# Optimization experiments

Measured on AMD Instinct MI355X. Metric: run time of the kernel, lower is better.

The kernel has to match this reference:

```python
import jax, jax.numpy as jnp
import numpy as np

EPS = 1e-05
B, T, F = 16, 2048, 768


def setup_inputs() -> dict:
    key = jax.random.key(0)
    k1, k2 = jax.random.split(key)
    input_values = jax.random.normal(k1, (B, T, F), dtype=jnp.float32)
    attention_mask = jax.random.randint(k2, (B, T), 0, 2, dtype=jnp.int32)
    return {"input_values": input_values, "attention_mask": attention_mask}


def _gauss_noise(shape):
    # mirrors _get_gauss_noise: scale randn into [0,1], then eps*((1-9)*g + 9)
    g = jax.random.normal(jax.random.key(42), shape, dtype=jnp.float32)
    g = g - jnp.min(g)
    g = g / jnp.max(g)
    return EPS * ((1.0 - 9.0) * g + 9.0)


def reference(input_values, attention_mask):
    x = input_values  # [B, T, F]
    Bx, Tx, Fx = x.shape
    # per-sample valid prefix length, as in the torch loop (vectorized)
    seq_lens = jnp.sum(attention_mask, axis=1).astype(jnp.float32)        # [B]
    rel = seq_lens / jnp.max(seq_lens)                                    # [B]
    actual = jnp.round(rel * Tx).astype(jnp.int32)                        # [B]
    # prefix mask over time: token t valid iff t < actual[b]
    m = (jnp.arange(Tx)[None, :] < actual[:, None]).astype(x.dtype)       # [B, T]
    cnt = actual.astype(x.dtype)[:, None]                                 # [B, 1]
    xm = x * m[:, :, None]
    mean = jnp.sum(xm, axis=1) / cnt                                      # [B, F]
    diff = (x - mean[:, None, :]) * m[:, :, None]
    # torch.std default: unbiased (ddof=1)
    std = jnp.sqrt(jnp.sum(diff * diff, axis=1) / (cnt - 1.0))            # [B, F]
    mean = mean + _gauss_noise(mean.shape)
    std = std + EPS
    pooled = jnp.concatenate([mean, std], axis=1)                         # [B, 2F]
    return pooled[:, None, :]                                             # [B, 1, 2F]
```

## Files before the change

kernel.cpp:

```cpp
#include <hip/hip_runtime.h>
#include <hip/hip_bf16.h>

#define B 16
#define T 2048
#define F 768
#define F4 (F / 4)
#define EPS 1e-5f
#define TS 64
#define TCHUNK (T / TS)


__global__ __launch_bounds__(1024) void k_actual(const int* __restrict__ mask,
                                                 int* __restrict__ actual) {
    __shared__ float slen[B];
    const int wave = threadIdx.x >> 6;
    const int lane = threadIdx.x & 63;
    int s = 0;
    const int* row = mask + wave * T;
    for (int t = lane; t < T; t += 64) s += row[t];
    for (int off = 32; off > 0; off >>= 1) s += __shfl_down(s, off, 64);
    if (lane == 0) slen[wave] = (float)s;
    __syncthreads();
    if (threadIdx.x < B) {
        float m = 0.f;
        for (int i = 0; i < B; i++) m = fmaxf(m, slen[i]);
        float rel = slen[threadIdx.x] / m;
        actual[threadIdx.x] = (int)rintf(rel * (float)T);
    }
}

__global__ __launch_bounds__(192) void k_partial(const float4* __restrict__ x,
                                                 const int* __restrict__ actual,
                                                 float* __restrict__ sum,
                                                 float* __restrict__ sumsq) {
    const int b = blockIdx.y;
    const int tstart = blockIdx.x * TCHUNK;
    const int tend = min(tstart + TCHUNK, actual[b]);
    const int tid = threadIdx.x;
    const float4* xb = x + (size_t)b * T * F4;

    float4 s = make_float4(0.f, 0.f, 0.f, 0.f);
    float4 q = make_float4(0.f, 0.f, 0.f, 0.f);
    for (int t = tstart; t < tend; ++t) {
        float4 v = xb[(size_t)t * F4 + tid];
        s.x += v.x; s.y += v.y; s.z += v.z; s.w += v.w;
        q.x += v.x * v.x; q.y += v.y * v.y; q.z += v.z * v.z; q.w += v.w * v.w;
    }
    if (tend > tstart) {
        const int base = b * F + 4 * tid;
        atomicAdd(&sum[base + 0], s.x);
        atomicAdd(&sum[base + 1], s.y);
        atomicAdd(&sum[base + 2], s.z);
        atomicAdd(&sum[base + 3], s.w);
        atomicAdd(&sumsq[base + 0], q.x);
        atomicAdd(&sumsq[base + 1], q.y);
        atomicAdd(&sumsq[base + 2], q.z);
        atomicAdd(&sumsq[base + 3], q.w);
    }
}

__global__ __launch_bounds__(256) void k_final(const float* __restrict__ sum,
                                               const float* __restrict__ sumsq,
                                               const int* __restrict__ actual,
                                               float* __restrict__ out) {
    const int idx = blockIdx.x * 256 + threadIdx.x;
    if (idx >= B * F) return;
    const int b = idx / F;
    const int f = idx - b * F;
    const float cnt = (float)actual[b];
    const float s = sum[idx];
    const float q = sumsq[idx];
    const float mean = s / cnt;
    float var = (q - s * s / cnt) / (cnt - 1.f);
    var = fmaxf(var, 0.f);
    out[b * 2 * F + f]     = mean;
    out[b * 2 * F + F + f] = sqrtf(var) + EPS;
}

extern "C" void kernel_launch(void* const* d_in, const int* in_sizes, int n_in,
                              void* d_out, int out_size, void* d_ws, size_t ws_size,
                              hipStream_t stream) {
    const float* x   = (const float*)d_in[0];
    const int* mask  = (const int*)d_in[1];
    float* out       = (float*)d_out;

    float* sum   = (float*)d_ws;
    float* sumsq = sum + B * F;
    int* actual  = (int*)(sumsq + B * F);

    hipMemsetAsync(d_ws, 0, (size_t)(2 * B * F) * sizeof(float), stream);

    k_actual<<<1, 1024, 0, stream>>>(mask, actual);
    k_partial<<<dim3(TS, B), 192, 0, stream>>>((const float4*)x, actual, sum, sumsq);
    k_final<<<(B * F + 255) / 256, 256, 0, stream>>>(sum, sumsq, actual, out);
}
```

Before: 170.0 us.

## Fuse mask-length computation into partial kernel and replace atomics with partial buffers

Drops the separate k_actual kernel and the memset. Each partial block now recomputes all 16 sequence lengths from the mask itself (128 KB read per block, mostly served from cache). The float atomics are replaced by plain per-tile partial-sum writes, and k_final reduces over the 64 tiles. This removes two launches and the atomic contention, in exchange for redundant mask reads in every block and an extra 2×64×B×F partial buffer that has to be written and read back.

Result: slower. 209.5 us (+23.2%).

```diff
diff --git a/kernel.cpp b/kernel.cpp
--- a/kernel.cpp
+++ b/kernel.cpp
@@ -8,35 +8,47 @@
 #define EPS 1e-5f
 #define TS 64
 #define TCHUNK (T / TS)
+#define NTHR 192
 
 
-__global__ __launch_bounds__(1024) void k_actual(const int* __restrict__ mask,
-                                                 int* __restrict__ actual) {
-    __shared__ float slen[B];
-    const int wave = threadIdx.x >> 6;
-    const int lane = threadIdx.x & 63;
-    int s = 0;
-    const int* row = mask + wave * T;
-    for (int t = lane; t < T; t += 64) s += row[t];
-    for (int off = 32; off > 0; off >>= 1) s += __shfl_down(s, off, 64);
-    if (lane == 0) slen[wave] = (float)s;
-    __syncthreads();
-    if (threadIdx.x < B) {
-        float m = 0.f;
-        for (int i = 0; i < B; i++) m = fmaxf(m, slen[i]);
-        float rel = slen[threadIdx.x] / m;
-        actual[threadIdx.x] = (int)rintf(rel * (float)T);
+__global__ __launch_bounds__(NTHR) void k_partial(const float4* __restrict__ x,
+                                                  const int* __restrict__ mask,
+                                                  float4* __restrict__ psum,
+                                                  float4* __restrict__ psq,
+                                                  int* __restrict__ actual_out) {
+    const int b    = blockIdx.y;
+    const int tile = blockIdx.x;
+    const int tid  = threadIdx.x;
+
+    __shared__ int red[12][16];
+    __shared__ int s_actual;
+    {
+        const int r = tid & 15;
+        const int j = tid >> 4;
+        int acc = 0;
+        const int* mrow = mask + r * T;
+        for (int t = j; t < T; t += 12) acc += mrow[t];
+        red[j][r] = acc;
+        __syncthreads();
+        if (tid < 16) {
+            int s = 0;
+            for (int j2 = 0; j2 < 12; j2++) s += red[j2][tid];
+            red[0][tid] = s;
+        }
+        __syncthreads();
+        if (tid == 0) {
+            float mx = 0.f;
+            for (int i = 0; i < B; i++) mx = fmaxf(mx, (float)red[0][i]);
+            float rel = (float)red[0][b] / mx;
+            s_actual = (int)rintf(rel * (float)T);
+        }
+        __syncthreads();
     }
-}
+    const int actual = s_actual;
+    if (tile == 0 && tid == 0) actual_out[b] = actual;
 
-__global__ __launch_bounds__(192) void k_partial(const float4* __restrict__ x,
-                                                 const int* __restrict__ actual,
-                                                 float* __restrict__ sum,
-                                                 float* __restrict__ sumsq) {
-    const int b = blockIdx.y;
-    const int tstart = blockIdx.x * TCHUNK;
-    const int tend = min(tstart + TCHUNK, actual[b]);
-    const int tid = threadIdx.x;
+    const int tstart = tile * TCHUNK;
+    const int tend   = min(tstart + TCHUNK, actual);
     const float4* xb = x + (size_t)b * T * F4;
 
     float4 s = make_float4(0.f, 0.f, 0.f, 0.f);
@@ -46,30 +58,25 @@
         s.x += v.x; s.y += v.y; s.z += v.z; s.w += v.w;
         q.x += v.x * v.x; q.y += v.y * v.y; q.z += v.z * v.z; q.w += v.w * v.w;
     }
-    if (tend > tstart) {
-        const int base = b * F + 4 * tid;
-        atomicAdd(&sum[base + 0], s.x);
-        atomicAdd(&sum[base + 1], s.y);
-        atomicAdd(&sum[base + 2], s.z);
-        atomicAdd(&sum[base + 3], s.w);
-        atomicAdd(&sumsq[base + 0], q.x);
-        atomicAdd(&sumsq[base + 1], q.y);
-        atomicAdd(&sumsq[base + 2], q.z);
-        atomicAdd(&sumsq[base + 3], q.w);
-    }
+    const size_t o = (size_t)(tile * B + b) * F4 + tid;
+    psum[o] = s;
+    psq[o]  = q;
 }
 
-__global__ __launch_bounds__(256) void k_final(const float* __restrict__ sum,
-                                               const float* __restrict__ sumsq,
+__global__ __launch_bounds__(256) void k_final(const float* __restrict__ psum,
+                                               const float* __restrict__ psq,
                                                const int* __restrict__ actual,
                                                float* __restrict__ out) {
     const int idx = blockIdx.x * 256 + threadIdx.x;
     if (idx >= B * F) return;
     const int b = idx / F;
     const int f = idx - b * F;
+    float s = 0.f, q = 0.f;
+    for (int tile = 0; tile < TS; ++tile) {
+        s += psum[(size_t)tile * B * F + idx];
+        q += psq [(size_t)tile * B * F + idx];
+    }
     const float cnt = (float)actual[b];
-    const float s = sum[idx];
-    const float q = sumsq[idx];
     const float mean = s / cnt;
     float var = (q - s * s / cnt) / (cnt - 1.f);
     var = fmaxf(var, 0.f);
@@ -80,17 +87,15 @@
 extern "C" void kernel_launch(void* const* d_in, const int* in_sizes, int n_in,
                               void* d_out, int out_size, void* d_ws, size_t ws_size,
                               hipStream_t stream) {
-    const float* x   = (const float*)d_in[0];
-    const int* mask  = (const int*)d_in[1];
-    float* out       = (float*)d_out;
+    const float* x  = (const float*)d_in[0];
+    const int* mask = (const int*)d_in[1];
+    float* out      = (float*)d_out;
 
-    float* sum   = (float*)d_ws;
-    float* sumsq = sum + B * F;
-    int* actual  = (int*)(sumsq + B * F);
+    float* psum = (float*)d_ws;
+    float* psq  = psum + (size_t)TS * B * F;
+    int* actual = (int*)(psq + (size_t)TS * B * F);
 
-    hipMemsetAsync(d_ws, 0, (size_t)(2 * B * F) * sizeof(float), stream);
-
-    k_actual<<<1, 1024, 0, stream>>>(mask, actual);
-    k_partial<<<dim3(TS, B), 192, 0, stream>>>((const float4*)x, actual, sum, sumsq);
-    k_final<<<(B * F + 255) / 256, 256, 0, stream>>>(sum, sumsq, actual, out);
+    k_partial<<<dim3(TS, B), NTHR, 0, stream>>>((const float4*)x, mask,
+                                                (float4*)psum, (float4*)psq, actual);
+    k_final<<<(B * F + 255) / 256, 256, 0, stream>>>(psum, psq, actual, out);
 }
```
